# Kernel optimization log

Hardware: AMD Instinct MI355X
Metric: run time of the kernel (lower is better)

## Reference

```python
import jax, jax.numpy as jnp
import numpy as np

N_NODES = 1048576
N_EDGES = 4 * N_NODES

def _mlp(h, w1, b1, w2, b2):
    return jax.nn.relu(h @ w1 + b1) @ w2 + b2

def setup_inputs() -> dict:
    key = jax.random.key(0)
    ks = jax.random.split(key, 12)
    def glorot(k, shape):
        fan_in, fan_out = shape
        lim = np.sqrt(6.0 / (fan_in + fan_out)).astype(np.float32)
        return jax.random.uniform(k, shape, jnp.float32, -lim, lim)
    x = jax.random.normal(ks[0], (N_NODES, 3), jnp.float32)
    edge_index = jax.random.randint(ks[1], (2, N_EDGES), 0, N_NODES, jnp.int64 if jax.config.jax_enable_x64 else jnp.int32)
    edge_attr = jax.random.normal(ks[2], (N_EDGES, 1), jnp.float32)
    u = jax.random.normal(ks[3], (1, 3), jnp.float32)
    batch = jnp.zeros((N_NODES,), jnp.int32)
    return {
        'x': x, 'edge_index': edge_index, 'edge_attr': edge_attr, 'u': u, 'batch': batch,
        'w1a': glorot(ks[4], (4, 20)), 'b1a': jnp.zeros((20,), jnp.float32),
        'w1b': glorot(ks[5], (20, 3)), 'b1b': jnp.zeros((3,), jnp.float32),
        'w2a': glorot(ks[6], (6, 20)), 'b2a': jnp.zeros((20,), jnp.float32),
        'w2b': glorot(ks[7], (20, 3)), 'b2b': jnp.zeros((3,), jnp.float32),
    }

def reference(x, edge_index, edge_attr, u, batch, w1a, b1a, w1b, b1b, w2a, b2a, w2b, b2b):
    row, col = edge_index[0], edge_index[1]
    n = x.shape[0]
    # gather source node feats, concat edge attr -> [E,4]
    h = jnp.concatenate([x[row], edge_attr], axis=1)
    h = _mlp(h, w1a, b1a, w1b, b1b)                    # [E,3]
    # scatter-mean over destination nodes
    s = jax.ops.segment_sum(h, col, num_segments=n)    # [N,3]
    cnt = jax.ops.segment_sum(jnp.ones((h.shape[0],), h.dtype), col, num_segments=n)
    agg = s / jnp.maximum(cnt, 1.0)[:, None]
    out = _mlp(jnp.concatenate([x, agg], axis=1), w2a, b2a, w2b, b2b)  # [N,3]
    fac = jnp.sqrt(jnp.sum(out ** 2, axis=1, keepdims=True))
    return out / fac
```

## Files before the change

### kernel.cpp

```cpp
#include <hip/hip_runtime.h>


#define SEG  4096
#define P1BT 256
#define P1BI (SEG / P1BT)
#define BKSH 12
#define BKN  4096
#define NBK  256
#define PFXW 257
#define P2T  1024

union HCvt { _Float16 h; unsigned short u; };

__device__ __forceinline__ float h2f(unsigned short u) {
    HCvt c; c.u = u; return (float)c.h;
}

__device__ __forceinline__ void mlp1_eval(
    float in0, float in1, float in2, float in3,
    const float* sw1a, const float* sb1a, const float* sw1b, const float* sb1b,
    float& o0, float& o1, float& o2)
{
    float h1[20];
#pragma unroll
    for (int j = 0; j < 20; ++j) {
        float v = sb1a[j];
        v = fmaf(in0, sw1a[0 * 20 + j], v);
        v = fmaf(in1, sw1a[1 * 20 + j], v);
        v = fmaf(in2, sw1a[2 * 20 + j], v);
        v = fmaf(in3, sw1a[3 * 20 + j], v);
        h1[j] = v > 0.f ? v : 0.f;
    }
    o0 = sb1b[0]; o1 = sb1b[1]; o2 = sb1b[2];
#pragma unroll
    for (int j = 0; j < 20; ++j) {
        o0 = fmaf(h1[j], sw1b[j * 3 + 0], o0);
        o1 = fmaf(h1[j], sw1b[j * 3 + 1], o1);
        o2 = fmaf(h1[j], sw1b[j * 3 + 2], o2);
    }
    o0 = fminf(fmaxf(o0, -8.0f), 8.0f - 2.0f / 2048.0f);
    o1 = fminf(fmaxf(o1, -8.0f), 8.0f - 2.0f / 2048.0f);
    o2 = fminf(fmaxf(o2, -8.0f), 8.0f - 2.0f / 1024.0f);
}

__device__ __forceinline__ unsigned long long payload_pack(float o0, float o1, float o2)
{
    const unsigned long long q0 = (unsigned int)__float2int_rn((o0 + 8.0f) * 2048.0f);
    const unsigned long long q1 = (unsigned int)__float2int_rn((o1 + 8.0f) * 2048.0f);
    const unsigned long long q2 = (unsigned int)__float2int_rn((o2 + 8.0f) * 1024.0f);
    return (q0 << 12) | (q1 << 27) | (q2 << 42);
}

__device__ __forceinline__ unsigned long long acc_pack(float o0, float o1, float o2)
{
    const unsigned long long q0 = (unsigned int)__float2int_rn((o0 + 8.0f) * 2048.0f);
    const unsigned long long q1 = (unsigned int)__float2int_rn((o1 + 8.0f) * 2048.0f);
    const unsigned long long q2 = (unsigned int)__float2int_rn((o2 + 8.0f) * 1024.0f);
    return 1ULL | (q0 << 5) | (q1 << 25) | (q2 << 45);
}

__device__ __forceinline__ void mlp2_store(
    unsigned long long q, const float* __restrict__ x, float* __restrict__ out,
    int n, const float* sw2a, const float* sb2a, const float* sw2b, const float* sb2b)
{
    const float cnt = (float)(unsigned int)(q & 31ULL);
    const float f0 = (float)(unsigned int)((q >> 5)  & 0xFFFFFULL);
    const float f1 = (float)(unsigned int)((q >> 25) & 0xFFFFFULL);
    const float f2 = (float)(unsigned int)(q >> 45);
    const float s0 = f0 * (1.0f / 2048.0f) - 8.0f * cnt;
    const float s1 = f1 * (1.0f / 2048.0f) - 8.0f * cnt;
    const float s2 = f2 * (1.0f / 1024.0f) - 8.0f * cnt;
    const float invc = 1.0f / fmaxf(cnt, 1.0f);

    const float in0 = x[n * 3 + 0];
    const float in1 = x[n * 3 + 1];
    const float in2 = x[n * 3 + 2];
    const float in3 = s0 * invc;
    const float in4 = s1 * invc;
    const float in5 = s2 * invc;

    float h1[20];
#pragma unroll
    for (int j = 0; j < 20; ++j) {
        float v = sb2a[j];
        v = fmaf(in0, sw2a[0 * 20 + j], v);
        v = fmaf(in1, sw2a[1 * 20 + j], v);
        v = fmaf(in2, sw2a[2 * 20 + j], v);
        v = fmaf(in3, sw2a[3 * 20 + j], v);
        v = fmaf(in4, sw2a[4 * 20 + j], v);
        v = fmaf(in5, sw2a[5 * 20 + j], v);
        h1[j] = v > 0.f ? v : 0.f;
    }
    float o0 = sb2b[0], o1 = sb2b[1], o2 = sb2b[2];
#pragma unroll
    for (int j = 0; j < 20; ++j) {
        o0 = fmaf(h1[j], sw2b[j * 3 + 0], o0);
        o1 = fmaf(h1[j], sw2b[j * 3 + 1], o1);
        o2 = fmaf(h1[j], sw2b[j * 3 + 2], o2);
    }
    const float inv = 1.0f / sqrtf(o0 * o0 + o1 * o1 + o2 * o2);
    out[n * 3 + 0] = o0 * inv;
    out[n * 3 + 1] = o1 * inv;
    out[n * 3 + 2] = o2 * inv;
}

__global__ __launch_bounds__(256) void pack_x_kernel(
    const float* __restrict__ x, ushort4* __restrict__ xp, int N)
{
    const int n = blockIdx.x * 256 + threadIdx.x;
    if (n >= N) return;
    HCvt c0, c1, c2;
    c0.h = (_Float16)x[n * 3 + 0];
    c1.h = (_Float16)x[n * 3 + 1];
    c2.h = (_Float16)x[n * 3 + 2];
    ushort4 r; r.x = c0.u; r.y = c1.u; r.z = c2.u; r.w = 0;
    xp[n] = r;
}

__global__ __launch_bounds__(256) void p1a_kernel(
    const ushort4* __restrict__ xp,
    const int*   __restrict__ edge_index,
    const float* __restrict__ edge_attr,
    const float* __restrict__ w1a, const float* __restrict__ b1a,
    const float* __restrict__ w1b, const float* __restrict__ b1b,
    unsigned long long* __restrict__ recs,
    int E)
{
    __shared__ float sw1a[80], sb1a[20], sw1b[60], sb1b[3];
    const int t = threadIdx.x;
    if (t < 80) sw1a[t] = w1a[t];
    if (t < 20) sb1a[t] = b1a[t];
    if (t < 60) sw1b[t] = w1b[t];
    if (t < 3)  sb1b[t] = b1b[t];
    __syncthreads();

    const int e = blockIdx.x * 256 + t;
    if (e >= E) return;

    const int row = edge_index[e];
    const float attr = edge_attr[e];
    const ushort4 px = xp[row];
    float o0, o1, o2;
    mlp1_eval(h2f(px.x), h2f(px.y), h2f(px.z), attr,
              sw1a, sb1a, sw1b, sb1b, o0, o1, o2);
    recs[e] = payload_pack(o0, o1, o2);
}

__global__ __launch_bounds__(P1BT) void p1b_kernel(
    const int* __restrict__ edge_index,
    unsigned long long* __restrict__ recs,
    unsigned short* __restrict__ pfx_tr,
    int E, int nsegs)
{
    __shared__ unsigned int hist[NBK];
    __shared__ unsigned int sc[NBK];
    __shared__ unsigned int pfx[PFXW];
    __shared__ __align__(16) unsigned long long svals[SEG];
    const int t = threadIdx.x;
    hist[t] = 0;
    __syncthreads();

    const int s = blockIdx.x;
    const int base = s * SEG;

    unsigned int col8[P1BI];
#pragma unroll
    for (int i = 0; i < P1BI; ++i) {
        const int e = base + i * P1BT + t;
        if (e < E) {
            const unsigned int c = (unsigned int)edge_index[E + e];
            col8[i] = c;
            atomicAdd(&hist[c >> BKSH], 1u);
        } else {
            col8[i] = 0xFFFFFFFFu;
        }
    }
    __syncthreads();

    sc[t] = hist[t];
    __syncthreads();
#pragma unroll
    for (int off = 1; off < NBK; off <<= 1) {
        const unsigned int u = (t >= off) ? sc[t - off] : 0u;
        __syncthreads();
        sc[t] += u;
        __syncthreads();
    }
    pfx[t + 1] = sc[t];
    if (t == 0) pfx[0] = 0;
    hist[t] = 0;
    __syncthreads();

    pfx_tr[(size_t)t * nsegs + s] = (unsigned short)pfx[t];
    if (t == 0) pfx_tr[(size_t)NBK * nsegs + s] = (unsigned short)pfx[NBK];

#pragma unroll
    for (int i = 0; i < P1BI; ++i) {
        const unsigned int c = col8[i];
        if (c == 0xFFFFFFFFu) continue;
        const int e = base + i * P1BT + t;
        const unsigned long long rec =
            recs[e] | (unsigned long long)(c & (BKN - 1));
        const unsigned int bkt = c >> BKSH;
        const unsigned int r = atomicAdd(&hist[bkt], 1u);
        svals[pfx[bkt] + r] = rec;
    }
    __syncthreads();

    unsigned long long* gv = recs + (size_t)base;
#pragma unroll
    for (int k = t; k < SEG; k += P1BT) gv[k] = svals[k];
}

__global__ __launch_bounds__(P2T) void p2_kernel(
    const float* __restrict__ x,
    const unsigned short* __restrict__ pfx_tr,
    const unsigned long long* __restrict__ vals,
    const float* __restrict__ w2a, const float* __restrict__ b2a,
    const float* __restrict__ w2b, const float* __restrict__ b2b,
    float* __restrict__ out,
    int N, int nsegs)
{
    __shared__ float sw2a[120], sb2a[20], sw2b[60], sb2b[3];
    __shared__ unsigned long long acc[BKN];
    const int t = threadIdx.x;
    if (t < 120) sw2a[t] = w2a[t];
    if (t < 20)  sb2a[t] = b2a[t];
    if (t < 60)  sw2b[t] = w2b[t];
    if (t < 3)   sb2b[t] = b2b[t];
#pragma unroll
    for (int k = 0; k < BKN / P2T; ++k) acc[k * P2T + t] = 0ULL;
    __syncthreads();

    const int b = blockIdx.x;
    const int wave = t >> 6;
    const int lane = t & 63;
    const int sub  = lane >> 4;
    const int sl   = lane & 15;
    const unsigned short* rowa = pfx_tr + (size_t)b * nsegs;
    const unsigned short* rowb = pfx_tr + (size_t)(b + 1) * nsegs;

    for (int sg = wave * 4; sg < nsegs; sg += (P2T / 64) * 4) {
        const int s = sg + sub;
        if (s < nsegs) {
            const unsigned int pa = rowa[s];
            const unsigned int pb = rowb[s];
            const size_t base = (size_t)s * SEG;
            for (unsigned int i = pa + sl; i < pb; i += 16) {
                const unsigned long long rec = vals[base + i];
                const unsigned int c = (unsigned int)(rec & 0xFFFULL);
                const unsigned long long q0 = (rec >> 12) & 0x7FFFULL;
                const unsigned long long q1 = (rec >> 27) & 0x7FFFULL;
                const unsigned long long q2 = (rec >> 42) & 0x3FFFULL;
                const unsigned long long add =
                    1ULL | (q0 << 5) | (q1 << 25) | (q2 << 45);
                atomicAdd(&acc[c], add);
            }
        }
    }
    __syncthreads();

    const int node0 = b * BKN;
#pragma unroll
    for (int k = 0; k < BKN / P2T; ++k) {
        const int n = node0 + k * P2T + t;
        if (n >= N) continue;
        mlp2_store(acc[k * P2T + t], x, out, n, sw2a, sb2a, sw2b, sb2b);
    }
}

__global__ __launch_bounds__(256) void edge_kernel_fb(
    const float* __restrict__ x, const int* __restrict__ edge_index,
    const float* __restrict__ edge_attr,
    const float* __restrict__ w1a, const float* __restrict__ b1a,
    const float* __restrict__ w1b, const float* __restrict__ b1b,
    unsigned long long* __restrict__ acc, int E)
{
    __shared__ float sw1a[80], sb1a[20], sw1b[60], sb1b[3];
    const int t = threadIdx.x;
    if (t < 80) sw1a[t] = w1a[t];
    if (t < 20) sb1a[t] = b1a[t];
    if (t < 60) sw1b[t] = w1b[t];
    if (t < 3)  sb1b[t] = b1b[t];
    __syncthreads();
    const int e = blockIdx.x * 256 + t;
    if (e >= E) return;
    const int row = edge_index[e];
    const int col = edge_index[E + e];
    float o0, o1, o2;
    mlp1_eval(x[row * 3 + 0], x[row * 3 + 1], x[row * 3 + 2], edge_attr[e],
              sw1a, sb1a, sw1b, sb1b, o0, o1, o2);
    atomicAdd(acc + col, acc_pack(o0, o1, o2));
}

__global__ __launch_bounds__(256) void node_kernel_fb(
    const float* __restrict__ x, const unsigned long long* __restrict__ acc,
    const float* __restrict__ w2a, const float* __restrict__ b2a,
    const float* __restrict__ w2b, const float* __restrict__ b2b,
    float* __restrict__ out, int N)
{
    __shared__ float sw2a[120], sb2a[20], sw2b[60], sb2b[3];
    const int t = threadIdx.x;
    if (t < 120) sw2a[t] = w2a[t];
    if (t < 20)  sb2a[t] = b2a[t];
    if (t < 60)  sw2b[t] = w2b[t];
    if (t < 3)   sb2b[t] = b2b[t];
    __syncthreads();
    const int n = blockIdx.x * 256 + t;
    if (n >= N) return;
    mlp2_store(acc[n], x, out, n, sw2a, sb2a, sw2b, sb2b);
}

extern "C" void kernel_launch(void* const* d_in, const int* in_sizes, int n_in,
                              void* d_out, int out_size, void* d_ws, size_t ws_size,
                              hipStream_t stream) {
    const float* x          = (const float*)d_in[0];
    const int*   edge_index = (const int*)  d_in[1];
    const float* edge_attr  = (const float*)d_in[2];
    const float* w1a = (const float*)d_in[5];
    const float* b1a = (const float*)d_in[6];
    const float* w1b = (const float*)d_in[7];
    const float* b1b = (const float*)d_in[8];
    const float* w2a = (const float*)d_in[9];
    const float* b2a = (const float*)d_in[10];
    const float* w2b = (const float*)d_in[11];
    const float* b2b = (const float*)d_in[12];

    const int N = in_sizes[0] / 3;
    const int E = in_sizes[2];

    const int nbuckets = (N + BKN - 1) / BKN;
    const int nsegs = (E + SEG - 1) / SEG;

    const size_t xp_bytes   = (size_t)N * sizeof(ushort4);
    const size_t recs_off   = (xp_bytes + 255) & ~(size_t)255;
    const size_t recs_bytes = (size_t)nsegs * SEG * sizeof(unsigned long long);
    const size_t pfx_off    = (recs_off + recs_bytes + 255) & ~(size_t)255;
    const size_t need       = pfx_off + (size_t)PFXW * nsegs * sizeof(unsigned short);

    const bool fast = (nbuckets <= NBK) && (ws_size >= need);

    if (fast) {
        ushort4* xp = (ushort4*)d_ws;
        unsigned long long* recs = (unsigned long long*)((char*)d_ws + recs_off);
        unsigned short* pfx_tr = (unsigned short*)((char*)d_ws + pfx_off);

        pack_x_kernel<<<(N + 255) / 256, 256, 0, stream>>>(x, xp, N);

        p1a_kernel<<<(E + 255) / 256, 256, 0, stream>>>(
            xp, edge_index, edge_attr, w1a, b1a, w1b, b1b, recs, E);

        p1b_kernel<<<nsegs, P1BT, 0, stream>>>(
            edge_index, recs, pfx_tr, E, nsegs);

        p2_kernel<<<nbuckets, P2T, 0, stream>>>(
            x, pfx_tr, recs, w2a, b2a, w2b, b2b, (float*)d_out, N, nsegs);
    } else {
        unsigned long long* acc = (unsigned long long*)d_ws;
        hipMemsetAsync(acc, 0, (size_t)N * sizeof(unsigned long long), stream);
        edge_kernel_fb<<<(E + 255) / 256, 256, 0, stream>>>(
            x, edge_index, edge_attr, w1a, b1a, w1b, b1b, acc, E);
        node_kernel_fb<<<(N + 255) / 256, 256, 0, stream>>>(
            x, acc, w2a, b2a, w2b, b2b, (float*)d_out, N);
    }
}
```

Before: 221.6 us.

## Halve destination bucket size, widen partition blocks, use wave-shuffle scan and nontemporal I/O

Destination buckets shrink from 4096 to 2048 nodes, giving 512 buckets. This doubles the number of aggregation blocks and halves their shared-memory accumulator. The partition kernel moves to 1024 threads and replaces its barrier-heavy shared-memory Hillis-Steele scan with wave-level shuffle scans plus a small serial combine. Streaming edge, record and prefix traffic switches to nontemporal loads and stores, with 128-bit vector writeback. The aggregation kernel uses 8-lane subgroups per segment instead of 16, and the larger prefix table means each aggregation block scans more entries.

```diff
diff --git a/kernel.cpp b/kernel.cpp
--- a/kernel.cpp
+++ b/kernel.cpp
@@ -2,13 +2,15 @@
 
 
 #define SEG  4096
-#define P1BT 256
+#define P1BT 1024
 #define P1BI (SEG / P1BT)
-#define BKSH 12
-#define BKN  4096
-#define NBK  256
-#define PFXW 257
+#define BKSH 11
+#define BKN  2048
+#define NBK  512
+#define PFXW (NBK + 1)
 #define P2T  1024
+
+typedef unsigned long long u64x2 __attribute__((ext_vector_type(2)));
 
 union HCvt { _Float16 h; unsigned short u; };
 
@@ -118,7 +120,7 @@
 }
 
 __global__ __launch_bounds__(256) void p1a_kernel(
-    const ushort4* __restrict__ xp,
+    const unsigned long long* __restrict__ xp,
     const int*   __restrict__ edge_index,
     const float* __restrict__ edge_attr,
     const float* __restrict__ w1a, const float* __restrict__ b1a,
@@ -137,13 +139,14 @@
     const int e = blockIdx.x * 256 + t;
     if (e >= E) return;
 
-    const int row = edge_index[e];
-    const float attr = edge_attr[e];
-    const ushort4 px = xp[row];
+    const int row = __builtin_nontemporal_load(edge_index + e);
+    const float attr = __builtin_nontemporal_load(edge_attr + e);
+    const unsigned long long px = xp[row];
     float o0, o1, o2;
-    mlp1_eval(h2f(px.x), h2f(px.y), h2f(px.z), attr,
+    mlp1_eval(h2f((unsigned short)px), h2f((unsigned short)(px >> 16)),
+              h2f((unsigned short)(px >> 32)), attr,
               sw1a, sb1a, sw1b, sb1b, o0, o1, o2);
-    recs[e] = payload_pack(o0, o1, o2);
+    __builtin_nontemporal_store(payload_pack(o0, o1, o2), recs + e);
 }
 
 __global__ __launch_bounds__(P1BT) void p1b_kernel(
@@ -153,63 +156,81 @@
     int E, int nsegs)
 {
     __shared__ unsigned int hist[NBK];
-    __shared__ unsigned int sc[NBK];
     __shared__ unsigned int pfx[PFXW];
+    __shared__ unsigned int wsum[NBK / 64];
     __shared__ __align__(16) unsigned long long svals[SEG];
     const int t = threadIdx.x;
-    hist[t] = 0;
+    if (t < NBK) hist[t] = 0;
     __syncthreads();
 
     const int s = blockIdx.x;
     const int base = s * SEG;
 
-    unsigned int col8[P1BI];
+    unsigned int col4[P1BI];
 #pragma unroll
     for (int i = 0; i < P1BI; ++i) {
         const int e = base + i * P1BT + t;
         if (e < E) {
-            const unsigned int c = (unsigned int)edge_index[E + e];
-            col8[i] = c;
+            const unsigned int c =
+                (unsigned int)__builtin_nontemporal_load(edge_index + E + e);
+            col4[i] = c;
             atomicAdd(&hist[c >> BKSH], 1u);
         } else {
-            col8[i] = 0xFFFFFFFFu;
+            col4[i] = 0xFFFFFFFFu;
         }
     }
     __syncthreads();
 
-    sc[t] = hist[t];
-    __syncthreads();
-#pragma unroll
-    for (int off = 1; off < NBK; off <<= 1) {
-        const unsigned int u = (t >= off) ? sc[t - off] : 0u;
-        __syncthreads();
-        sc[t] += u;
-        __syncthreads();
-    }
-    pfx[t + 1] = sc[t];
+    unsigned int inc = 0;
+    if (t < NBK) {
+        const int lane = t & 63;
+        unsigned int v = hist[t];
+#pragma unroll
+        for (int off = 1; off < 64; off <<= 1) {
+            const unsigned int u = __shfl_up(v, off);
+            if (lane >= off) v += u;
+        }
+        inc = v;
+        if (lane == 63) wsum[t >> 6] = v;
+    }
+    __syncthreads();
+    if (t == 0) {
+        unsigned int run = 0;
+#pragma unroll
+        for (int k = 0; k < NBK / 64; ++k) {
+            const unsigned int w = wsum[k]; wsum[k] = run; run += w;
+        }
+    }
+    __syncthreads();
+    if (t < NBK) {
+        pfx[t + 1] = inc + wsum[t >> 6];
+        hist[t] = 0;
+    }
     if (t == 0) pfx[0] = 0;
-    hist[t] = 0;
-    __syncthreads();
-
-    pfx_tr[(size_t)t * nsegs + s] = (unsigned short)pfx[t];
-    if (t == 0) pfx_tr[(size_t)NBK * nsegs + s] = (unsigned short)pfx[NBK];
+    __syncthreads();
+
+    if (t < NBK) pfx_tr[(size_t)t * nsegs + s] = (unsigned short)pfx[t];
+    if (t == 0)  pfx_tr[(size_t)NBK * nsegs + s] = (unsigned short)pfx[NBK];
 
 #pragma unroll
     for (int i = 0; i < P1BI; ++i) {
-        const unsigned int c = col8[i];
+        const unsigned int c = col4[i];
         if (c == 0xFFFFFFFFu) continue;
         const int e = base + i * P1BT + t;
         const unsigned long long rec =
-            recs[e] | (unsigned long long)(c & (BKN - 1));
+            __builtin_nontemporal_load(recs + e) |
+            (unsigned long long)(c & (BKN - 1));
         const unsigned int bkt = c >> BKSH;
         const unsigned int r = atomicAdd(&hist[bkt], 1u);
         svals[pfx[bkt] + r] = rec;
     }
     __syncthreads();
 
-    unsigned long long* gv = recs + (size_t)base;
-#pragma unroll
-    for (int k = t; k < SEG; k += P1BT) gv[k] = svals[k];
+    u64x2* gv2 = (u64x2*)(recs + (size_t)base);
+    const u64x2* sv2 = (const u64x2*)svals;
+#pragma unroll
+    for (int k = t; k < SEG / 2; k += P1BT)
+        __builtin_nontemporal_store(sv2[k], gv2 + k);
 }
 
 __global__ __launch_bounds__(P2T) void p2_kernel(
@@ -235,19 +256,20 @@
     const int b = blockIdx.x;
     const int wave = t >> 6;
     const int lane = t & 63;
-    const int sub  = lane >> 4;
-    const int sl   = lane & 15;
+    const int sub  = lane >> 3;
+    const int sl   = lane & 7;
     const unsigned short* rowa = pfx_tr + (size_t)b * nsegs;
     const unsigned short* rowb = pfx_tr + (size_t)(b + 1) * nsegs;
 
-    for (int sg = wave * 4; sg < nsegs; sg += (P2T / 64) * 4) {
+    for (int sg = wave * 8; sg < nsegs; sg += (P2T / 64) * 8) {
         const int s = sg + sub;
         if (s < nsegs) {
             const unsigned int pa = rowa[s];
             const unsigned int pb = rowb[s];
             const size_t base = (size_t)s * SEG;
-            for (unsigned int i = pa + sl; i < pb; i += 16) {
-                const unsigned long long rec = vals[base + i];
+            for (unsigned int i = pa + sl; i < pb; i += 8) {
+                const unsigned long long rec =
+                    __builtin_nontemporal_load(vals + base + i);
                 const unsigned int c = (unsigned int)(rec & 0xFFFULL);
                 const unsigned long long q0 = (rec >> 12) & 0x7FFFULL;
                 const unsigned long long q1 = (rec >> 27) & 0x7FFFULL;
@@ -306,7 +328,7 @@
     if (t < 60)  sw2b[t] = w2b[t];
     if (t < 3)   sb2b[t] = b2b[t];
     __syncthreads();
-    const int n = blockIdx.x * 256 + t;
+    const int n = blockIdx.x * 256 + threadIdx.x;
     if (n >= N) return;
     mlp2_store(acc[n], x, out, n, sw2a, sb2a, sw2b, sb2b);
 }
@@ -332,7 +354,7 @@
     const int nbuckets = (N + BKN - 1) / BKN;
     const int nsegs = (E + SEG - 1) / SEG;
 
-    const size_t xp_bytes   = (size_t)N * sizeof(ushort4);
+    const size_t xp_bytes   = (size_t)N * sizeof(unsigned long long);
     const size_t recs_off   = (xp_bytes + 255) & ~(size_t)255;
     const size_t recs_bytes = (size_t)nsegs * SEG * sizeof(unsigned long long);
     const size_t pfx_off    = (recs_off + recs_bytes + 255) & ~(size_t)255;
@@ -341,11 +363,12 @@
     const bool fast = (nbuckets <= NBK) && (ws_size >= need);
 
     if (fast) {
-        ushort4* xp = (ushort4*)d_ws;
+        unsigned long long* xp = (unsigned long long*)d_ws;
         unsigned long long* recs = (unsigned long long*)((char*)d_ws + recs_off);
         unsigned short* pfx_tr = (unsigned short*)((char*)d_ws + pfx_off);
 
-        pack_x_kernel<<<(N + 255) / 256, 256, 0, stream>>>(x, xp, N);
+        pack_x_kernel<<<(N + 255) / 256, 256, 0, stream>>>(
+            x, (ushort4*)xp, N);
 
         p1a_kernel<<<(E + 255) / 256, 256, 0, stream>>>(
             xp, edge_index, edge_attr, w1a, b1a, w1b, b1b, recs, E);
```

After: 235.1 us. +6.1%, slower.
